# Performance work log

Measured on AMD Instinct MI355X. Metric: run time of the kernel, lower is better.

## Reference

```python
import jax, jax.numpy as jnp
import numpy as np

N_NODES = 1_000_000
N_GRAPHS = 20_000
C, M, N_GEN = 10, 50, 8


def setup_inputs() -> dict:
    key = jax.random.key(0)
    k1, k2, k3, k4 = jax.random.split(key, 4)
    x = jax.random.randint(k1, (N_NODES,), 0, M, dtype=jnp.int64 if jax.config.jax_enable_x64 else jnp.int32)
    batch = jnp.sort(jax.random.randint(k2, (N_NODES,), 0, N_GRAPHS, dtype=jnp.int64 if jax.config.jax_enable_x64 else jnp.int32))
    B = jax.random.normal(k3, (C, M, N_GEN), dtype=jnp.float32) * 2.0
    Pi = jax.random.normal(k4, (C, N_GEN), dtype=jnp.float32) * 2.0
    return {"x": x, "batch": batch, "B": B, "Pi": Pi}


def reference(x, batch, B, Pi):
    # softmax reparameterization: per-generator softmax over M (for B) and over C (for Pi)
    sm_B = jax.nn.softmax(B, axis=1)            # [C, M, n_gen]
    sm_Pi = jax.nn.softmax(Pi, axis=0)          # [C, n_gen]

    # gather emission probs for each node's label: sm_B[:, x] -> [C, N, n_gen] -> [N, C, n_gen]
    emit = jnp.transpose(jnp.take(sm_B, x, axis=1), (1, 0, 2))  # [N, C, n_gen]
    numerator = sm_Pi[None, :, :] * emit                        # [N, C, n_gen]

    posterior = numerator / jnp.sum(numerator, axis=1, keepdims=True)
    likelihood = jnp.sum(posterior * jnp.log(numerator), axis=1)  # [N, n_gen]

    # scatter-sum per graph
    likelihood = jax.ops.segment_sum(likelihood, batch, num_segments=N_GRAPHS)  # [G, n_gen]

    h_states = jnp.argmax(posterior, axis=1)  # [N, n_gen]
    return likelihood, h_states
```

## Files before the change

### kernel.cpp

```cpp
#include <hip/hip_runtime.h>

#define NN 1000000
#define NG 20000
#define C_ 10
#define M_ 50
#define G_ 8

typedef float f32x4 __attribute__((ext_vector_type(4)));

__global__ __launch_bounds__(256) void k_fused(const float* __restrict__ B,
                                               const float* __restrict__ Pi,
                                               const int* __restrict__ x,
                                               const int* __restrict__ batch,
                                               float* __restrict__ out,
                                               float* __restrict__ outh) {
    __shared__ float sZB[C_ * G_];
    __shared__ float sZP[G_];
    __shared__ float lik[M_ * 9];
    __shared__ unsigned int hpack[M_];
    __shared__ int sx[1024];
    __shared__ int sb[1025];

    const int t = threadIdx.x;
    const int lane = t & 63;
    const int w = t >> 6;
    const int base = blockIdx.x * 1024;
    const int limit = (NN - base < 1024) ? (NN - base) : 1024;

    const int vdet = x[2 * lane + 1] | x[128 + 2 * lane + 1];
    const int is64 = (__ballot(vdet != 0) == 0ULL) ? 1 : 0;

    if (is64) {
        const int4* xq = (const int4*)x + (base >> 1);
        const int4* bq = (const int4*)batch + (base >> 1);
        for (int i = t; i < (limit >> 1); i += 256) {
            const int4 a = xq[i];
            sx[2 * i] = a.x; sx[2 * i + 1] = a.z;
            const int4 b2 = bq[i];
            sb[1 + 2 * i] = b2.x; sb[2 + 2 * i] = b2.z;
        }
        if (t == 0) sb[0] = (base == 0) ? -1 : batch[2 * (base - 1)];
    } else {
        const int4* xq = (const int4*)x + (base >> 2);
        const int4* bq = (const int4*)batch + (base >> 2);
        for (int i = t; i < (limit >> 2); i += 256) {
            const int4 a = xq[i];
            sx[4 * i] = a.x; sx[4 * i + 1] = a.y; sx[4 * i + 2] = a.z; sx[4 * i + 3] = a.w;
            const int4 b2 = bq[i];
            sb[1 + 4 * i] = b2.x; sb[2 + 4 * i] = b2.y; sb[3 + 4 * i] = b2.z; sb[4 + 4 * i] = b2.w;
        }
        if (t == 0) sb[0] = (base == 0) ? -1 : batch[base - 1];
    }

    if (t < 80) {
        const int c = t >> 3, g = t & 7;
        float Z = 0.f;
        for (int m = 0; m < M_; ++m) Z += __expf(B[(c * M_ + m) * G_ + g]);
        sZB[t] = __logf(Z);
    } else if (t < 88) {
        const int g = t - 80;
        float Z = 0.f;
        for (int c = 0; c < C_; ++c) Z += __expf(Pi[c * G_ + g]);
        sZP[g] = __logf(Z);
    }
    __syncthreads();

    for (int e = t; e < M_ * G_; e += 256) {
        const int m = e >> 3, g = e & 7;
        float s[C_];
        float bv = -1e30f;
        int bi = 0;
        for (int c = 0; c < C_; ++c) {
            const float v = (B[(c * M_ + m) * G_ + g] - sZB[c * G_ + g]) +
                            (Pi[c * G_ + g] - sZP[g]);
            s[c] = v;
            if (v > bv) { bv = v; bi = c; }
        }
        float Z = 0.f, W = 0.f;
        for (int c = 0; c < C_; ++c) {
            const float ee = __expf(s[c]);
            Z += ee;
            W += ee * s[c];
        }
        lik[m * 9 + g] = W / Z;
        unsigned int pk = 0;
#pragma unroll
        for (int g2 = 0; g2 < 8; ++g2)
            pk |= ((unsigned)__shfl(bi, (lane & ~7) + g2, 64) & 15u) << (4 * g2);
        if ((t & 7) == 0) hpack[m] = pk;
    }
    __syncthreads();

    for (int rr = 0; rr < 4; ++rr) {
        const int ib = 256 * w + 64 * rr;
        const int i = ib + lane;
        const bool head = (i < limit) && (sb[1 + i] != sb[i]);
        unsigned long long hm = __ballot(head);
        while (hm) {
            const int i0 = ib + (int)__builtin_ctzll(hm);
            hm &= hm - 1;
            const int g  = sb[1 + i0];
            const int gp = sb[i0];
            if (lane < 8)
                for (int gg = gp + 1; gg < g; ++gg)
                    out[(size_t)gg * 8 + lane] = 0.f;

            const int n0 = base + i0;
            int n_end = NN;
            for (int bse = n0; ; bse += 64) {
                const int ii = bse + lane;
                int val = g + 1;
                if (ii < NN)
                    val = (ii < base + limit) ? sb[1 + ii - base]
                                              : (is64 ? batch[2 * (size_t)ii] : batch[ii]);
                const unsigned long long diff = __ballot(val != g);
                if (diff) { n_end = bse + (int)__builtin_ctzll(diff); break; }
            }

            const int ns = lane >> 3, r = lane & 7;
            float acc = 0.f;
            for (int n = n0 + ns; n < n_end; n += 8) {
                const int xi = (n < base + limit) ? sx[n - base]
                                                  : (is64 ? x[2 * (size_t)n] : x[n]);
                acc += lik[xi * 9 + r];
            }
            acc += __shfl_xor(acc, 8, 64);
            acc += __shfl_xor(acc, 16, 64);
            acc += __shfl_xor(acc, 32, 64);
            if (lane < 8) out[(size_t)g * 8 + lane] = acc;

            if (n_end == NN && lane < 8)
                for (int gg = g + 1; gg < NG; ++gg)
                    out[(size_t)gg * 8 + lane] = 0.f;
        }
    }

    f32x4* op = (f32x4*)outh + (size_t)base * 2;
    const int nf4 = limit * 2;
    for (int idx = t; idx < nf4; idx += 256) {
        const unsigned int pk = hpack[sx[idx >> 1]];
        const int sh = (idx & 1) * 16;
        f32x4 v;
        v.x = (float)((pk >> (sh + 0)) & 15u);
        v.y = (float)((pk >> (sh + 4)) & 15u);
        v.z = (float)((pk >> (sh + 8)) & 15u);
        v.w = (float)((pk >> (sh + 12)) & 15u);
        __builtin_nontemporal_store(v, &op[idx]);
    }
}

extern "C" void kernel_launch(void* const* d_in, const int* in_sizes, int n_in,
                              void* d_out, int out_size, void* d_ws, size_t ws_size,
                              hipStream_t stream) {
    const int*   x     = (const int*)d_in[0];
    const int*   batch = (const int*)d_in[1];
    const float* B     = (const float*)d_in[2];
    const float* Pi    = (const float*)d_in[3];
    float* out  = (float*)d_out;
    float* outh = (float*)d_out + NG * G_;

    k_fused<<<(NN + 1023) / 1024, 256, 0, stream>>>(B, Pi, x, batch, out, outh);
}
```

Measured before the change: 21.63 us.

## Halve per-block chunk, drop shared x staging, emit argmax output first

Shrinks each block's node chunk from 1024 to 512 so twice as many blocks launch. Node labels are no longer staged in shared memory and are read straight from global memory in both the argmax-output loop and the segment-sum loop. The argmax output store now runs before the segment scan, so the large writes start earlier. The trade-off is more blocks repeating the softmax table setup, and redundant global reads of x in place of one staged load.

```diff
diff --git a/kernel.cpp b/kernel.cpp
--- a/kernel.cpp
+++ b/kernel.cpp
@@ -5,6 +5,7 @@
 #define C_ 10
 #define M_ 50
 #define G_ 8
+#define CHUNK 512
 
 typedef float f32x4 __attribute__((ext_vector_type(4)));
 
@@ -18,39 +19,33 @@
     __shared__ float sZP[G_];
     __shared__ float lik[M_ * 9];
     __shared__ unsigned int hpack[M_];
-    __shared__ int sx[1024];
-    __shared__ int sb[1025];
+    __shared__ int sb[CHUNK + 1];
 
     const int t = threadIdx.x;
     const int lane = t & 63;
     const int w = t >> 6;
-    const int base = blockIdx.x * 1024;
-    const int limit = (NN - base < 1024) ? (NN - base) : 1024;
+    const int base = blockIdx.x * CHUNK;
+    const int limit = (NN - base < CHUNK) ? (NN - base) : CHUNK;
 
     const int vdet = x[2 * lane + 1] | x[128 + 2 * lane + 1];
     const int is64 = (__ballot(vdet != 0) == 0ULL) ? 1 : 0;
 
     if (is64) {
-        const int4* xq = (const int4*)x + (base >> 1);
         const int4* bq = (const int4*)batch + (base >> 1);
         for (int i = t; i < (limit >> 1); i += 256) {
-            const int4 a = xq[i];
-            sx[2 * i] = a.x; sx[2 * i + 1] = a.z;
             const int4 b2 = bq[i];
             sb[1 + 2 * i] = b2.x; sb[2 + 2 * i] = b2.z;
         }
-        if (t == 0) sb[0] = (base == 0) ? -1 : batch[2 * (base - 1)];
     } else {
-        const int4* xq = (const int4*)x + (base >> 2);
         const int4* bq = (const int4*)batch + (base >> 2);
         for (int i = t; i < (limit >> 2); i += 256) {
-            const int4 a = xq[i];
-            sx[4 * i] = a.x; sx[4 * i + 1] = a.y; sx[4 * i + 2] = a.z; sx[4 * i + 3] = a.w;
             const int4 b2 = bq[i];
-            sb[1 + 4 * i] = b2.x; sb[2 + 4 * i] = b2.y; sb[3 + 4 * i] = b2.z; sb[4 + 4 * i] = b2.w;
+            sb[1 + 4 * i] = b2.x; sb[2 + 4 * i] = b2.y;
+            sb[3 + 4 * i] = b2.z; sb[4 + 4 * i] = b2.w;
         }
-        if (t == 0) sb[0] = (base == 0) ? -1 : batch[base - 1];
     }
+    if (t == 0)
+        sb[0] = (base == 0) ? -1 : (is64 ? batch[2 * (base - 1)] : batch[base - 1]);
 
     if (t < 80) {
         const int c = t >> 3, g = t & 7;
@@ -91,8 +86,24 @@
     }
     __syncthreads();
 
-    for (int rr = 0; rr < 4; ++rr) {
-        const int ib = 256 * w + 64 * rr;
+    f32x4* op = (f32x4*)outh + (size_t)base * 2;
+    const int nf4 = limit * 2;
+#pragma unroll 4
+    for (int idx = t; idx < nf4; idx += 256) {
+        const int n = base + (idx >> 1);
+        const int xi = is64 ? x[2 * (size_t)n] : x[n];
+        const unsigned int pk = hpack[xi];
+        const int sh = (idx & 1) * 16;
+        f32x4 v;
+        v.x = (float)((pk >> (sh + 0)) & 15u);
+        v.y = (float)((pk >> (sh + 4)) & 15u);
+        v.z = (float)((pk >> (sh + 8)) & 15u);
+        v.w = (float)((pk >> (sh + 12)) & 15u);
+        __builtin_nontemporal_store(v, &op[idx]);
+    }
+
+    for (int rr = 0; rr < CHUNK / 4 / 64; ++rr) {
+        const int ib = (CHUNK / 4) * w + 64 * rr;
         const int i = ib + lane;
         const bool head = (i < limit) && (sb[1 + i] != sb[i]);
         unsigned long long hm = __ballot(head);
@@ -120,8 +131,7 @@
             const int ns = lane >> 3, r = lane & 7;
             float acc = 0.f;
             for (int n = n0 + ns; n < n_end; n += 8) {
-                const int xi = (n < base + limit) ? sx[n - base]
-                                                  : (is64 ? x[2 * (size_t)n] : x[n]);
+                const int xi = is64 ? x[2 * (size_t)n] : x[n];
                 acc += lik[xi * 9 + r];
             }
             acc += __shfl_xor(acc, 8, 64);
@@ -133,19 +143,6 @@
                 for (int gg = g + 1; gg < NG; ++gg)
                     out[(size_t)gg * 8 + lane] = 0.f;
         }
-    }
-
-    f32x4* op = (f32x4*)outh + (size_t)base * 2;
-    const int nf4 = limit * 2;
-    for (int idx = t; idx < nf4; idx += 256) {
-        const unsigned int pk = hpack[sx[idx >> 1]];
-        const int sh = (idx & 1) * 16;
-        f32x4 v;
-        v.x = (float)((pk >> (sh + 0)) & 15u);
-        v.y = (float)((pk >> (sh + 4)) & 15u);
-        v.z = (float)((pk >> (sh + 8)) & 15u);
-        v.w = (float)((pk >> (sh + 12)) & 15u);
-        __builtin_nontemporal_store(v, &op[idx]);
     }
 }
 
@@ -159,5 +156,5 @@
     float* out  = (float*)d_out;
     float* outh = (float*)d_out + NG * G_;
 
-    k_fused<<<(NN + 1023) / 1024, 256, 0, stream>>>(B, Pi, x, batch, out, outh);
+    k_fused<<<(NN + CHUNK - 1) / CHUNK, 256, 0, stream>>>(B, Pi, x, batch, out, outh);
 }
```

New measurement: 24.02 us. 11.0% more time.
